# Optimization experiments

Hardware: AMD Instinct MI355X
Metric: run time of the kernel (lower is better)

The kernel has to match this reference:

```python
import jax, jax.numpy as jnp
import numpy as np

B, S, D, H, E, K = 1, 4096, 1024, 4096, 8, 2


def setup_inputs() -> dict:
    key = jax.random.key(0)
    ks = jax.random.split(key, 10)
    scale = 0.02
    return {
        "hidden_states": jax.random.normal(ks[0], (B, S, D), dtype=jnp.float32),
        "gate_w": jax.random.normal(ks[1], (E, D), dtype=jnp.float32) * scale,
        "w_in": jax.random.normal(ks[2], (E, D, H), dtype=jnp.float32) * scale,
        "b_in": jnp.zeros((E, H), dtype=jnp.float32),
        "w_out": jax.random.normal(ks[3], (E, H, D), dtype=jnp.float32) * scale,
        "b_out": jnp.zeros((E, D), dtype=jnp.float32),
        "sw_in": jax.random.normal(ks[4], (D, H), dtype=jnp.float32) * scale,
        "sb_in": jnp.zeros((H,), dtype=jnp.float32),
        "sw_out": jax.random.normal(ks[5], (H, D), dtype=jnp.float32) * scale,
        "sb_out": jnp.zeros((D,), dtype=jnp.float32),
    }


def _ffn(x, w1, b1, w2, b2):
    # Linear -> exact (erf) GELU -> Linear, matching torch F.gelu default
    h = jax.nn.gelu(x @ w1 + b1, approximate=False)
    return h @ w2 + b2


def reference(hidden_states, gate_w, w_in, b_in, w_out, b_out,
              sw_in, sb_in, sw_out, sb_out):
    orig_shape = hidden_states.shape
    d = orig_shape[-1]
    x = hidden_states.reshape(-1, d)            # [T, D]
    T = x.shape[0]
    n_exp = gate_w.shape[0]

    # --- MoE gate: softmax over expert logits, top-k (sorted flag irrelevant
    # since the combine below is order-invariant) ---
    scores = jax.nn.softmax(x @ gate_w.T, axis=-1)        # [T, E]
    topk_w, topk_idx = jax.lax.top_k(scores, K)           # [T, K]

    # Per-token dense combine weights: w_tok[t, e] = sum of topk weights routed to e
    w_tok = jnp.zeros((T, n_exp), dtype=x.dtype).at[
        jnp.arange(T)[:, None], topk_idx].add(topk_w)     # [T, E]

    # --- expert dispatch + weighted combine (loop over small fixed E) ---
    y = jnp.zeros_like(x)
    for e in range(n_exp):
        y = y + w_tok[:, e:e + 1] * _ffn(x, w_in[e], b_in[e], w_out[e], b_out[e])

    # --- shared expert on the full (unflattened) input ---
    shared = _ffn(hidden_states, sw_in, sb_in, sw_out, sb_out)
    return y.reshape(orig_shape) + shared
```

## Files before the change

### kernel.cpp

```cpp
#include <hip/hip_runtime.h>
#include <hip/hip_bf16.h>
#include <math.h>


typedef unsigned short ushort_t;
typedef __attribute__((ext_vector_type(8))) __bf16 bf16x8;
typedef __attribute__((ext_vector_type(4))) float f32x4;

#define T_TOK 4096
#define DDIM  1024
#define HDIM  4096
#define NEXP  8
#define SLOT_MAX 9216

#define OFF_TIDX  0u
#define OFF_TW    32768u
#define OFF_OFFS  65536u
#define OFF_SLOT  65792u
#define OFF_TOK   98560u
#define OFF_XG    262144u
#define OFF_XB    (OFF_XG + 18874368u)
#define OFF_W     (OFF_XB + 8388608u)
#define OFF_SW2   (OFF_W + 33554432u)
#define OFF_H     (OFF_W + 67108864u)
#define OFF_OUTS  (OFF_H + 75497472u)

__device__ __forceinline__ ushort_t f2b(float f) {
    __hip_bfloat16 h = __float2bfloat16(f);
    return *reinterpret_cast<ushort_t*>(&h);
}
__device__ __forceinline__ float b2f(ushort_t u) {
    __hip_bfloat16 h;
    *reinterpret_cast<ushort_t*>(&h) = u;
    return __bfloat162float(h);
}
__device__ __forceinline__ float gelu_exact(float v) {
    return 0.5f * v * (1.0f + erff(v * 0.70710678118654752f));
}

__global__ void gate_kernel(const float* __restrict__ x, const float* __restrict__ gw,
                            int* __restrict__ tidx, float* __restrict__ tw) {
    int t = blockIdx.x;
    int l = threadIdx.x;
    float acc[NEXP];
#pragma unroll
    for (int e = 0; e < NEXP; ++e) acc[e] = 0.f;
    for (int i = 0; i < DDIM / 64; ++i) {
        float xi = x[(size_t)t * DDIM + i * 64 + l];
#pragma unroll
        for (int e = 0; e < NEXP; ++e)
            acc[e] += xi * gw[e * DDIM + i * 64 + l];
    }
#pragma unroll
    for (int e = 0; e < NEXP; ++e)
        for (int off = 32; off; off >>= 1) acc[e] += __shfl_xor(acc[e], off);
    if (l == 0) {
        float m = acc[0];
#pragma unroll
        for (int e = 1; e < NEXP; ++e) m = fmaxf(m, acc[e]);
        float ex[NEXP], Z = 0.f;
#pragma unroll
        for (int e = 0; e < NEXP; ++e) { ex[e] = __expf(acc[e] - m); Z += ex[e]; }
        int b0 = 0;
#pragma unroll
        for (int e = 1; e < NEXP; ++e) if (ex[e] > ex[b0]) b0 = e;
        int b1 = (b0 == 0) ? 1 : 0;
#pragma unroll
        for (int e = 0; e < NEXP; ++e) if (e != b0 && ex[e] > ex[b1]) b1 = e;
        float inv = 1.0f / Z;
        tidx[2 * t] = b0; tidx[2 * t + 1] = b1;
        tw[2 * t] = ex[b0] * inv; tw[2 * t + 1] = ex[b1] * inv;
    }
}

__global__ void scan_kernel(const int* __restrict__ tidx, int* __restrict__ offs,
                            int* __restrict__ slot_of, int* __restrict__ tok_of) {
    int lane = threadIdx.x;
    int cnt[NEXP];
#pragma unroll
    for (int e = 0; e < NEXP; ++e) cnt[e] = 0;
    for (int base = 0; base < 2 * T_TOK; base += 64) {
        int v = tidx[base + lane];
#pragma unroll
        for (int e = 0; e < NEXP; ++e)
            cnt[e] += __popcll(__ballot(v == e));
    }
    int off[NEXP + 1];
    off[0] = 0;
#pragma unroll
    for (int e = 0; e < NEXP; ++e) off[e + 1] = off[e] + ((cnt[e] + 127) & ~127);
    if (lane == 0) {
#pragma unroll
        for (int e = 0; e <= NEXP; ++e) offs[e] = off[e];
    }
    int run[NEXP];
#pragma unroll
    for (int e = 0; e < NEXP; ++e) run[e] = off[e];
    unsigned long long mylow = (lane == 0) ? 0ull : ((~0ull) >> (64 - lane));
    for (int base = 0; base < 2 * T_TOK; base += 64) {
        int v = tidx[base + lane];
#pragma unroll
        for (int e = 0; e < NEXP; ++e) {
            unsigned long long m = __ballot(v == e);
            if (v == e) {
                int s = run[e] + __popcll(m & mylow);
                slot_of[base + lane] = s;
                tok_of[s] = (base + lane) >> 1;
            }
            run[e] += __popcll(m);
        }
    }
#pragma unroll
    for (int e = 0; e < NEXP; ++e)
        for (int s = run[e] + lane; s < off[e + 1]; s += 64) tok_of[s] = -1;
}

__global__ void build_x(const float* __restrict__ x, const int* __restrict__ tok_of,
                        const int* __restrict__ offs, ushort_t* __restrict__ Xg,
                        ushort_t* __restrict__ Xb) {
    int b = blockIdx.x;
    int k = threadIdx.x * 4;
    if (b < SLOT_MAX) {
        if (b >= offs[NEXP]) return;
        int t = tok_of[b];
        float4 v = make_float4(0.f, 0.f, 0.f, 0.f);
        if (t >= 0) v = *(const float4*)(x + (size_t)t * DDIM + k);
        ushort_t* p = Xg + (size_t)b * DDIM + k;
        p[0] = f2b(v.x); p[1] = f2b(v.y); p[2] = f2b(v.z); p[3] = f2b(v.w);
    } else {
        int row = b - SLOT_MAX;
        float4 v = *(const float4*)(x + (size_t)row * DDIM + k);
        ushort_t* p = Xb + (size_t)row * DDIM + k;
        p[0] = f2b(v.x); p[1] = f2b(v.y); p[2] = f2b(v.z); p[3] = f2b(v.w);
    }
}

__global__ void transpose_cvt(const float* __restrict__ in, ushort_t* __restrict__ out,
                              int K, int N) {
    __shared__ float t[64][65];
    size_t zoff = (size_t)blockIdx.z * K * N;
    in += zoff; out += zoff;
    int k0 = blockIdx.x * 64, n0 = blockIdx.y * 64;
    int c = threadIdx.x & 63, r4 = threadIdx.x >> 6;
#pragma unroll
    for (int i = 0; i < 16; ++i) {
        int r = r4 + i * 4;
        t[r][c] = in[(size_t)(k0 + r) * N + n0 + c];
    }
    __syncthreads();
#pragma unroll
    for (int i = 0; i < 16; ++i) {
        int r = r4 + i * 4;
        out[(size_t)(n0 + r) * K + k0 + c] = f2b(t[c][r]);
    }
}

template <bool EXPERT, bool ACT_GELU, bool OUT_BF16>
__global__ __launch_bounds__(256) void gemm_bt(
    const ushort_t* __restrict__ A, const ushort_t* __restrict__ BtBase,
    const float* __restrict__ biasBase, void* __restrict__ Cout,
    const int* __restrict__ offs, int N, int K) {
    int m0 = blockIdx.x * 128, n0 = blockIdx.y * 128;
    const ushort_t* Bt = BtBase;
    const float* bias = biasBase;
    if (EXPERT) {
        int total = offs[NEXP];
        if (m0 >= total) return;
        int e = 0;
        while (offs[e + 1] <= m0) e++;
        Bt = BtBase + (size_t)e * N * K;
        bias = biasBase + (size_t)e * N;
    }

    __shared__ ushort_t As[128 * 64];
    __shared__ ushort_t Bs[128 * 64];

    int tid = threadIdx.x;
    int lane = tid & 63, wid = tid >> 6;
    int wm = wid >> 1, wn = wid & 1;
    int q = lane >> 4, lr = lane & 15;

    size_t Aoff[4], Boff[4];
    int ldsOff[4];
#pragma unroll
    for (int it = 0; it < 4; ++it) {
        int row = it * 32 + (tid >> 3);
        int c = (tid & 7) ^ (row & 7);
        Aoff[it] = (size_t)(m0 + row) * K + c * 8;
        Boff[it] = (size_t)(n0 + row) * K + c * 8;
        ldsOff[it] = (it * 256 + wid * 64) * 8;
    }

    int rowA[4], rowB[4];
#pragma unroll
    for (int i = 0; i < 4; ++i) {
        rowA[i] = wm * 64 + i * 16 + lr;
        rowB[i] = wn * 64 + i * 16 + lr;
    }

    f32x4 acc[4][4];
#pragma unroll
    for (int i = 0; i < 4; ++i)
#pragma unroll
        for (int j = 0; j < 4; ++j) acc[i][j] = (f32x4)(0.f);

    for (int kb = 0; kb < K; kb += 64) {
#pragma unroll
        for (int it = 0; it < 4; ++it) {
            __builtin_amdgcn_global_load_lds(
                (const __attribute__((address_space(1))) void*)(A + Aoff[it] + kb),
                (__attribute__((address_space(3))) void*)(As + ldsOff[it]), 16, 0, 0);
            __builtin_amdgcn_global_load_lds(
                (const __attribute__((address_space(1))) void*)(Bt + Boff[it] + kb),
                (__attribute__((address_space(3))) void*)(Bs + ldsOff[it]), 16, 0, 0);
        }
        __syncthreads();
#pragma unroll
        for (int ks = 0; ks < 2; ++ks) {
            bf16x8 af[4], bfr[4];
#pragma unroll
            for (int i = 0; i < 4; ++i) {
                int cA = (ks * 4 + q) ^ (rowA[i] & 7);
                af[i] = *(const bf16x8*)(As + rowA[i] * 64 + cA * 8);
                int cB = (ks * 4 + q) ^ (rowB[i] & 7);
                bfr[i] = *(const bf16x8*)(Bs + rowB[i] * 64 + cB * 8);
            }
#pragma unroll
            for (int i = 0; i < 4; ++i)
#pragma unroll
                for (int j = 0; j < 4; ++j)
                    acc[i][j] = __builtin_amdgcn_mfma_f32_16x16x32_bf16(
                        af[i], bfr[j], acc[i][j], 0, 0, 0);
        }
        __syncthreads();
    }

    int colb = n0 + wn * 64 + lr;
    int rowb = m0 + wm * 64 + q * 4;
#pragma unroll
    for (int j = 0; j < 4; ++j) {
        int col = colb + j * 16;
        float bz = bias[col];
#pragma unroll
        for (int i = 0; i < 4; ++i) {
            int row = rowb + i * 16;
#pragma unroll
            for (int r = 0; r < 4; ++r) {
                float v = acc[i][j][r] + bz;
                if (ACT_GELU) v = gelu_exact(v);
                if (OUT_BF16)
                    ((ushort_t*)Cout)[(size_t)(row + r) * N + col] = f2b(v);
                else
                    ((float*)Cout)[(size_t)(row + r) * N + col] = v;
            }
        }
    }
}

__global__ void combine_kernel(float* __restrict__ out, const ushort_t* __restrict__ OutS,
                               const int* __restrict__ slot_of, const float* __restrict__ tw) {
    int t = blockIdx.x;
    int d = threadIdx.x * 4;
    int s0 = slot_of[2 * t], s1 = slot_of[2 * t + 1];
    float w0 = tw[2 * t], w1 = tw[2 * t + 1];
    float* po = out + (size_t)t * DDIM + d;
    float4 o = *(float4*)po;
    const ushort_t* p0 = OutS + (size_t)s0 * DDIM + d;
    const ushort_t* p1 = OutS + (size_t)s1 * DDIM + d;
    o.x += w0 * b2f(p0[0]) + w1 * b2f(p1[0]);
    o.y += w0 * b2f(p0[1]) + w1 * b2f(p1[1]);
    o.z += w0 * b2f(p0[2]) + w1 * b2f(p1[2]);
    o.w += w0 * b2f(p0[3]) + w1 * b2f(p1[3]);
    *(float4*)po = o;
}

extern "C" void kernel_launch(void* const* d_in, const int* in_sizes, int n_in,
                              void* d_out, int out_size, void* d_ws, size_t ws_size,
                              hipStream_t stream) {
    const float* x      = (const float*)d_in[0];
    const float* gw     = (const float*)d_in[1];
    const float* w_in   = (const float*)d_in[2];
    const float* b_in   = (const float*)d_in[3];
    const float* w_out  = (const float*)d_in[4];
    const float* b_out  = (const float*)d_in[5];
    const float* sw_in  = (const float*)d_in[6];
    const float* sb_in  = (const float*)d_in[7];
    const float* sw_out = (const float*)d_in[8];
    const float* sb_out = (const float*)d_in[9];
    float* out = (float*)d_out;

    char* ws = (char*)d_ws;
    int*      tidx    = (int*)(ws + OFF_TIDX);
    float*    tw      = (float*)(ws + OFF_TW);
    int*      offs    = (int*)(ws + OFF_OFFS);
    int*      slot_of = (int*)(ws + OFF_SLOT);
    int*      tok_of  = (int*)(ws + OFF_TOK);
    ushort_t* Xg      = (ushort_t*)(ws + OFF_XG);
    ushort_t* Xb      = (ushort_t*)(ws + OFF_XB);
    ushort_t* Wt      = (ushort_t*)(ws + OFF_W);
    ushort_t* SW2t    = (ushort_t*)(ws + OFF_SW2);
    ushort_t* Hbuf    = (ushort_t*)(ws + OFF_H);
    ushort_t* OutS    = (ushort_t*)(ws + OFF_OUTS);

    gate_kernel<<<T_TOK, 64, 0, stream>>>(x, gw, tidx, tw);
    scan_kernel<<<1, 64, 0, stream>>>(tidx, offs, slot_of, tok_of);
    build_x<<<SLOT_MAX + T_TOK, 256, 0, stream>>>(x, tok_of, offs, Xg, Xb);
    transpose_cvt<<<dim3(DDIM / 64, HDIM / 64, NEXP), 256, 0, stream>>>(w_in, Wt, DDIM, HDIM);
    gemm_bt<true, true, true><<<dim3(SLOT_MAX / 128, HDIM / 128), 256, 0, stream>>>(
        Xg, Wt, b_in, Hbuf, offs, HDIM, DDIM);
    transpose_cvt<<<dim3(HDIM / 64, DDIM / 64, NEXP), 256, 0, stream>>>(w_out, Wt, HDIM, DDIM);
    gemm_bt<true, false, true><<<dim3(SLOT_MAX / 128, DDIM / 128), 256, 0, stream>>>(
        Hbuf, Wt, b_out, OutS, offs, DDIM, HDIM);
    transpose_cvt<<<dim3(DDIM / 64, HDIM / 64, 1), 256, 0, stream>>>(sw_in, Wt, DDIM, HDIM);
    transpose_cvt<<<dim3(HDIM / 64, DDIM / 64, 1), 256, 0, stream>>>(sw_out, SW2t, HDIM, DDIM);
    gemm_bt<false, true, true><<<dim3(T_TOK / 128, HDIM / 128), 256, 0, stream>>>(
        Xb, Wt, sb_in, Hbuf, nullptr, HDIM, DDIM);
    gemm_bt<false, false, false><<<dim3(T_TOK / 128, DDIM / 128), 256, 0, stream>>>(
        Hbuf, SW2t, sb_out, out, nullptr, DDIM, HDIM);
    combine_kernel<<<T_TOK, 256, 0, stream>>>(out, OutS, slot_of, tw);
    (void)in_sizes; (void)n_in; (void)out_size; (void)ws_size;
}
```

Baseline: 686.7 us.

## Merge shared and routed expert GEMMs, double-buffer LDS, replace serial scan with atomics

Shared-expert rows are appended after the routed slots in one activation buffer, so each FFN layer runs as a single grouped GEMM launch with expert index 8 meaning the shared weights. The GEMM K-loop now double-buffers LDS tiles so global-to-LDS loads for the next k-block overlap MFMA compute. The single-wavefront scan is replaced by gate-time atomic counters, a tiny offsets kernel and a parallel atomic slot-assign kernel. Slot order within an expert becomes nondeterministic, and the doubled LDS footprint may reduce occupancy.

```diff
diff --git a/kernel.cpp b/kernel.cpp
--- a/kernel.cpp
+++ b/kernel.cpp
@@ -12,18 +12,18 @@
 #define HDIM  4096
 #define NEXP  8
 #define SLOT_MAX 9216
-
-#define OFF_TIDX  0u
-#define OFF_TW    32768u
-#define OFF_OFFS  65536u
+#define M_ALL (SLOT_MAX + T_TOK)
+
+#define OFF_CNT   0u
+#define OFF_OFFS  64u
+#define OFF_TIDX  256u
+#define OFF_TW    33024u
 #define OFF_SLOT  65792u
 #define OFF_TOK   98560u
-#define OFF_XG    262144u
-#define OFF_XB    (OFF_XG + 18874368u)
-#define OFF_W     (OFF_XB + 8388608u)
-#define OFF_SW2   (OFF_W + 33554432u)
-#define OFF_H     (OFF_W + 67108864u)
-#define OFF_OUTS  (OFF_H + 75497472u)
+#define OFF_XALL  1048576u
+#define OFF_OUTS  OFF_XALL
+#define OFF_WT    (OFF_XALL + 28311552u)
+#define OFF_H     (OFF_WT + 75497472u)
 
 __device__ __forceinline__ ushort_t f2b(float f) {
     __hip_bfloat16 h = __float2bfloat16(f);
@@ -38,8 +38,15 @@
     return 0.5f * v * (1.0f + erff(v * 0.70710678118654752f));
 }
 
+__global__ void init_kernel(int* __restrict__ cnt, int* __restrict__ tok_of) {
+    int i = blockIdx.x * 256 + threadIdx.x;
+    if (i < 16) cnt[i] = 0;
+    if (i < SLOT_MAX) tok_of[i] = -1;
+}
+
 __global__ void gate_kernel(const float* __restrict__ x, const float* __restrict__ gw,
-                            int* __restrict__ tidx, float* __restrict__ tw) {
+                            int* __restrict__ tidx, float* __restrict__ tw,
+                            int* __restrict__ cnt) {
     int t = blockIdx.x;
     int l = threadIdx.x;
     float acc[NEXP];
@@ -70,69 +77,49 @@
         float inv = 1.0f / Z;
         tidx[2 * t] = b0; tidx[2 * t + 1] = b1;
         tw[2 * t] = ex[b0] * inv; tw[2 * t + 1] = ex[b1] * inv;
-    }
-}
-
-__global__ void scan_kernel(const int* __restrict__ tidx, int* __restrict__ offs,
-                            int* __restrict__ slot_of, int* __restrict__ tok_of) {
-    int lane = threadIdx.x;
-    int cnt[NEXP];
-#pragma unroll
-    for (int e = 0; e < NEXP; ++e) cnt[e] = 0;
-    for (int base = 0; base < 2 * T_TOK; base += 64) {
-        int v = tidx[base + lane];
-#pragma unroll
-        for (int e = 0; e < NEXP; ++e)
-            cnt[e] += __popcll(__ballot(v == e));
-    }
-    int off[NEXP + 1];
-    off[0] = 0;
-#pragma unroll
-    for (int e = 0; e < NEXP; ++e) off[e + 1] = off[e] + ((cnt[e] + 127) & ~127);
-    if (lane == 0) {
-#pragma unroll
-        for (int e = 0; e <= NEXP; ++e) offs[e] = off[e];
-    }
-    int run[NEXP];
-#pragma unroll
-    for (int e = 0; e < NEXP; ++e) run[e] = off[e];
-    unsigned long long mylow = (lane == 0) ? 0ull : ((~0ull) >> (64 - lane));
-    for (int base = 0; base < 2 * T_TOK; base += 64) {
-        int v = tidx[base + lane];
+        atomicAdd(&cnt[b0], 1);
+        atomicAdd(&cnt[b1], 1);
+    }
+}
+
+__global__ void offs_kernel(const int* __restrict__ cnt, int* __restrict__ offs) {
+    if (threadIdx.x == 0 && blockIdx.x == 0) {
+        int o = 0;
 #pragma unroll
         for (int e = 0; e < NEXP; ++e) {
-            unsigned long long m = __ballot(v == e);
-            if (v == e) {
-                int s = run[e] + __popcll(m & mylow);
-                slot_of[base + lane] = s;
-                tok_of[s] = (base + lane) >> 1;
-            }
-            run[e] += __popcll(m);
+            offs[e] = o;
+            o += (cnt[e] + 127) & ~127;
         }
-    }
-#pragma unroll
-    for (int e = 0; e < NEXP; ++e)
-        for (int s = run[e] + lane; s < off[e + 1]; s += 64) tok_of[s] = -1;
+        offs[NEXP] = o;
+    }
+}
+
+__global__ void assign_kernel(const int* __restrict__ tidx, const int* __restrict__ offs,
+                              int* __restrict__ cur, int* __restrict__ slot_of,
+                              int* __restrict__ tok_of) {
+    int i = blockIdx.x * 256 + threadIdx.x;
+    if (i >= 2 * T_TOK) return;
+    int e = tidx[i];
+    int s = offs[e] + atomicAdd(&cur[e], 1);
+    slot_of[i] = s;
+    tok_of[s] = i >> 1;
 }
 
 __global__ void build_x(const float* __restrict__ x, const int* __restrict__ tok_of,
-                        const int* __restrict__ offs, ushort_t* __restrict__ Xg,
-                        ushort_t* __restrict__ Xb) {
+                        const int* __restrict__ offs, ushort_t* __restrict__ Xall) {
     int b = blockIdx.x;
     int k = threadIdx.x * 4;
+    int t;
     if (b < SLOT_MAX) {
         if (b >= offs[NEXP]) return;
-        int t = tok_of[b];
-        float4 v = make_float4(0.f, 0.f, 0.f, 0.f);
-        if (t >= 0) v = *(const float4*)(x + (size_t)t * DDIM + k);
-        ushort_t* p = Xg + (size_t)b * DDIM + k;
-        p[0] = f2b(v.x); p[1] = f2b(v.y); p[2] = f2b(v.z); p[3] = f2b(v.w);
+        t = tok_of[b];
     } else {
-        int row = b - SLOT_MAX;
-        float4 v = *(const float4*)(x + (size_t)row * DDIM + k);
-        ushort_t* p = Xb + (size_t)row * DDIM + k;
-        p[0] = f2b(v.x); p[1] = f2b(v.y); p[2] = f2b(v.z); p[3] = f2b(v.w);
-    }
+        t = b - SLOT_MAX;
+    }
+    float4 v = make_float4(0.f, 0.f, 0.f, 0.f);
+    if (t >= 0) v = *(const float4*)(x + (size_t)t * DDIM + k);
+    ushort_t* p = Xall + (size_t)b * DDIM + k;
+    p[0] = f2b(v.x); p[1] = f2b(v.y); p[2] = f2b(v.z); p[3] = f2b(v.w);
 }
 
 __global__ void transpose_cvt(const float* __restrict__ in, ushort_t* __restrict__ out,
@@ -155,25 +142,26 @@
     }
 }
 
-template <bool EXPERT, bool ACT_GELU, bool OUT_BF16>
-__global__ __launch_bounds__(256) void gemm_bt(
-    const ushort_t* __restrict__ A, const ushort_t* __restrict__ BtBase,
-    const float* __restrict__ biasBase, void* __restrict__ Cout,
+template <bool ACT_GELU, bool FFN2>
+__global__ __launch_bounds__(256) void gemm_moe(
+    const ushort_t* __restrict__ A, const ushort_t* __restrict__ WtBase,
+    const float* __restrict__ bExp, const float* __restrict__ bSh,
+    ushort_t* __restrict__ Cb, float* __restrict__ Cf,
     const int* __restrict__ offs, int N, int K) {
     int m0 = blockIdx.x * 128, n0 = blockIdx.y * 128;
-    const ushort_t* Bt = BtBase;
-    const float* bias = biasBase;
-    if (EXPERT) {
-        int total = offs[NEXP];
-        if (m0 >= total) return;
-        int e = 0;
+    int e;
+    if (m0 >= SLOT_MAX) {
+        e = NEXP;
+    } else {
+        if (m0 >= offs[NEXP]) return;
+        e = 0;
         while (offs[e + 1] <= m0) e++;
-        Bt = BtBase + (size_t)e * N * K;
-        bias = biasBase + (size_t)e * N;
-    }
-
-    __shared__ ushort_t As[128 * 64];
-    __shared__ ushort_t Bs[128 * 64];
+    }
+    const ushort_t* Bt = WtBase + (size_t)e * N * K;
+    const float* bias = (e == NEXP) ? bSh : bExp + (size_t)e * N;
+
+    __shared__ ushort_t As[2][128 * 64];
+    __shared__ ushort_t Bs[2][128 * 64];
 
     int tid = threadIdx.x;
     int lane = tid & 63, wid = tid >> 6;
@@ -204,26 +192,27 @@
 #pragma unroll
         for (int j = 0; j < 4; ++j) acc[i][j] = (f32x4)(0.f);
 
-    for (int kb = 0; kb < K; kb += 64) {
+    auto stage = [&](int kb, int buf) {
 #pragma unroll
         for (int it = 0; it < 4; ++it) {
             __builtin_amdgcn_global_load_lds(
                 (const __attribute__((address_space(1))) void*)(A + Aoff[it] + kb),
-                (__attribute__((address_space(3))) void*)(As + ldsOff[it]), 16, 0, 0);
+                (__attribute__((address_space(3))) void*)(&As[buf][ldsOff[it]]), 16, 0, 0);
             __builtin_amdgcn_global_load_lds(
                 (const __attribute__((address_space(1))) void*)(Bt + Boff[it] + kb),
-                (__attribute__((address_space(3))) void*)(Bs + ldsOff[it]), 16, 0, 0);
+                (__attribute__((address_space(3))) void*)(&Bs[buf][ldsOff[it]]), 16, 0, 0);
         }
-        __syncthreads();
+    };
+    auto compute = [&](int buf) {
 #pragma unroll
         for (int ks = 0; ks < 2; ++ks) {
             bf16x8 af[4], bfr[4];
 #pragma unroll
             for (int i = 0; i < 4; ++i) {
                 int cA = (ks * 4 + q) ^ (rowA[i] & 7);
-                af[i] = *(const bf16x8*)(As + rowA[i] * 64 + cA * 8);
+                af[i] = *(const bf16x8*)(&As[buf][rowA[i] * 64 + cA * 8]);
                 int cB = (ks * 4 + q) ^ (rowB[i] & 7);
-                bfr[i] = *(const bf16x8*)(Bs + rowB[i] * 64 + cB * 8);
+                bfr[i] = *(const bf16x8*)(&Bs[buf][rowB[i] * 64 + cB * 8]);
             }
 #pragma unroll
             for (int i = 0; i < 4; ++i)
@@ -232,7 +221,17 @@
                     acc[i][j] = __builtin_amdgcn_mfma_f32_16x16x32_bf16(
                         af[i], bfr[j], acc[i][j], 0, 0, 0);
         }
+    };
+
+    const int nk = K >> 6;
+    stage(0, 0);
+    __syncthreads();
+    int cur = 0;
+    for (int t = 0; t < nk; ++t) {
+        if (t + 1 < nk) stage((t + 1) << 6, cur ^ 1);
+        compute(cur);
         __syncthreads();
+        cur ^= 1;
     }
 
     int colb = n0 + wn * 64 + lr;
@@ -248,10 +247,10 @@
             for (int r = 0; r < 4; ++r) {
                 float v = acc[i][j][r] + bz;
                 if (ACT_GELU) v = gelu_exact(v);
-                if (OUT_BF16)
-                    ((ushort_t*)Cout)[(size_t)(row + r) * N + col] = f2b(v);
+                if (!FFN2 || e < NEXP)
+                    Cb[(size_t)(row + r) * N + col] = f2b(v);
                 else
-                    ((float*)Cout)[(size_t)(row + r) * N + col] = v;
+                    Cf[(size_t)(row + r - SLOT_MAX) * N + col] = v;
             }
         }
     }
@@ -290,33 +289,36 @@
     float* out = (float*)d_out;
 
     char* ws = (char*)d_ws;
+    int*      cnt     = (int*)(ws + OFF_CNT);
+    int*      offs    = (int*)(ws + OFF_OFFS);
     int*      tidx    = (int*)(ws + OFF_TIDX);
     float*    tw      = (float*)(ws + OFF_TW);
-    int*      offs    = (int*)(ws + OFF_OFFS);
     int*      slot_of = (int*)(ws + OFF_SLOT);
     int*      tok_of  = (int*)(ws + OFF_TOK);
-    ushort_t* Xg      = (ushort_t*)(ws + OFF_XG);
-    ushort_t* Xb      = (ushort_t*)(ws + OFF_XB);
-    ushort_t* Wt      = (ushort_t*)(ws + OFF_W);
-    ushort_t* SW2t    = (ushort_t*)(ws + OFF_SW2);
+    ushort_t* Xall    = (ushort_t*)(ws + OFF_XALL);
+    ushort_t* OutS    = (ushort_t*)(ws + OFF_OUTS);
+    ushort_t* Wt      = (ushort_t*)(ws + OFF_WT);
     ushort_t* Hbuf    = (ushort_t*)(ws + OFF_H);
-    ushort_t* OutS    = (ushort_t*)(ws + OFF_OUTS);
-
-    gate_kernel<<<T_TOK, 64, 0, stream>>>(x, gw, tidx, tw);
-    scan_kernel<<<1, 64, 0, stream>>>(tidx, offs, slot_of, tok_of);
-    build_x<<<SLOT_MAX + T_TOK, 256, 0, stream>>>(x, tok_of, offs, Xg, Xb);
+
+    init_kernel<<<(SLOT_MAX + 255) / 256, 256, 0, stream>>>(cnt, tok_of);
+    gate_kernel<<<T_TOK, 64, 0, stream>>>(x, gw, tidx, tw, cnt);
+    offs_kernel<<<1, 64, 0, stream>>>(cnt, offs);
+    assign_kernel<<<(2 * T_TOK + 255) / 256, 256, 0, stream>>>(tidx, offs, cnt + 8,
+                                                               slot_of, tok_of);
+    build_x<<<M_ALL, 256, 0, stream>>>(x, tok_of, offs, Xall);
+
     transpose_cvt<<<dim3(DDIM / 64, HDIM / 64, NEXP), 256, 0, stream>>>(w_in, Wt, DDIM, HDIM);
-    gemm_bt<true, true, true><<<dim3(SLOT_MAX / 128, HDIM / 128), 256, 0, stream>>>(
-        Xg, Wt, b_in, Hbuf, offs, HDIM, DDIM);
+    transpose_cvt<<<dim3(DDIM / 64, HDIM / 64, 1), 256, 0, stream>>>(
+        sw_in, Wt + (size_t)NEXP * HDIM * DDIM, DDIM, HDIM);
+    gemm_moe<true, false><<<dim3(M_ALL / 128, HDIM / 128), 256, 0, stream>>>(
+        Xall, Wt, b_in, sb_in, Hbuf, nullptr, offs, HDIM, DDIM);
+
     transpose_cvt<<<dim3(HDIM / 64, DDIM / 64, NEXP), 256, 0, stream>>>(w_out, Wt, HDIM, DDIM);
-    gemm_bt<true, false, true><<<dim3(SLOT_MAX / 128, DDIM / 128), 256, 0, stream>>>(
-        Hbuf, Wt, b_out, OutS, offs, DDIM, HDIM);
-    transpose_cvt<<<dim3(DDIM / 64, HDIM / 64, 1), 256, 0, stream>>>(sw_in, Wt, DDIM, HDIM);
-    transpose_cvt<<<dim3(HDIM / 64, DDIM / 64, 1), 256, 0, stream>>>(sw_out, SW2t, HDIM, DDIM);
-    gemm_bt<false, true, true><<<dim3(T_TOK / 128, HDIM / 128), 256, 0, stream>>>(
-        Xb, Wt, sb_in, Hbuf, nullptr, HDIM, DDIM);
-    gemm_bt<false, false, false><<<dim3(T_TOK / 128, DDIM / 128), 256, 0, stream>>>(
-        Hbuf, SW2t, sb_out, out, nullptr, DDIM, HDIM);
+    transpose_cvt<<<dim3(HDIM / 64, DDIM / 64, 1), 256, 0, stream>>>(
+        sw_out, Wt + (size_t)NEXP * HDIM * DDIM, HDIM, DDIM);
+    gemm_moe<false, true><<<dim3(M_ALL / 128, DDIM / 128), 256, 0, stream>>>(
+        Hbuf, Wt, b_out, sb_out, OutS, out, offs, DDIM, HDIM);
+
     combine_kernel<<<T_TOK, 256, 0, stream>>>(out, OutS, slot_of, tw);
     (void)in_sizes; (void)n_in; (void)out_size; (void)ws_size;
 }
```

After: 636.0 us. -7.4%, faster.
